# Optimization experiments

Hardware: AMD Instinct MI355X
Metric: run time of the kernel (lower is better)

The kernel has to match this reference:

```python
import jax, jax.numpy as jnp
import numpy as np

WS = 7          # window_size[0]
UP = 2          # hardcoded upscale
WS2 = WS * UP   # 14
NUM_HEADS = 6
DIM = 192
HEAD_DIM = DIM // NUM_HEADS
SCALE = HEAD_DIM ** -0.5
TABLE_SIZE = (WS + WS2 - 1) ** 2  # 400


def _relative_position_index():
    # Mirrors the torch __init__ index construction (meshgrid 'ij').
    ch = np.arange(WS)
    cw = np.arange(WS2)
    r1, c1 = np.meshgrid(ch, ch, indexing='ij')   # (7,7)
    r2, c2 = np.meshgrid(cw, cw, indexing='ij')   # (14,14)
    r1, c1 = r1.reshape(-1), c1.reshape(-1)       # (49,)
    r2, c2 = r2.reshape(-1), c2.reshape(-1)       # (196,)
    rel_row = r1[:, None] - r2[None, :] + (WS2 - 1)          # (49,196) in [0,19]
    rel_col = c1[:, None] - c2[None, :] + (WS2 - 1)
    idx = rel_row * (WS + WS2 - 1) + rel_col                 # (49,196) in [0,399]
    return jnp.asarray(idx, dtype=jnp.int32)

REL_INDEX = _relative_position_index()


def setup_inputs() -> dict:
    key = jax.random.key(0)
    ks = jax.random.split(key, 9)
    B, N, N2, C = 1024, WS * WS, WS2 * WS2, DIM
    std = 0.02
    return {
        'x1': jax.random.normal(ks[0], (B, N, C), jnp.float32),
        'x2': jax.random.normal(ks[1], (B, N2, C), jnp.float32),
        # Linear weights stored as (in, out) so y = x @ W + b
        'qkv_w': jax.random.normal(ks[2], (C, C), jnp.float32) * std,
        'qkv_b': jnp.zeros((C,), jnp.float32),
        'qkv2_w': jax.random.normal(ks[3], (C, 2 * C), jnp.float32) * std,
        'qkv2_b': jnp.zeros((2 * C,), jnp.float32),
        'proj_w': jax.random.normal(ks[4], (C, C), jnp.float32) * std,
        'proj_b': jnp.zeros((C,), jnp.float32),
        'bias_table': jax.random.normal(ks[5], (TABLE_SIZE, NUM_HEADS), jnp.float32) * std,
    }


def reference(x1, x2, qkv_w, qkv_b, qkv2_w, qkv2_b, proj_w, proj_b, bias_table):
    B, N, C = x1.shape
    _, N2, _ = x2.shape
    H, D = NUM_HEADS, HEAD_DIM

    q = (x1 @ qkv_w + qkv_b).reshape(B, N, H, D).transpose(0, 2, 1, 3)        # [B,H,N,D]
    kv = (x2 @ qkv2_w + qkv2_b).reshape(B, N2, 2, H, D).transpose(2, 0, 3, 1, 4)
    k, v = kv[0], kv[1]                                                        # [B,H,N2,D]

    attn = jnp.einsum('bhnd,bhmd->bhnm', q * SCALE, k)                         # [B,H,N,N2]
    bias = bias_table[REL_INDEX].transpose(2, 0, 1)                            # [H,N,N2]
    attn = jax.nn.softmax(attn + bias[None], axis=-1)

    out = jnp.einsum('bhnm,bhmd->bhnd', attn, v).transpose(0, 2, 1, 3).reshape(B, N, C)
    return out @ proj_w + proj_b
```

## Files before the change

### kernel.cpp

```cpp
#include <hip/hip_runtime.h>


typedef __attribute__((ext_vector_type(8))) short bf16x8;
typedef __attribute__((ext_vector_type(4))) float f32x4;

#define MFMA16(a, b, c) __builtin_amdgcn_mfma_f32_16x16x32_bf16((a), (b), (c), 0, 0, 0)

#define WS_QKVT  0
#define WS_QKV2T 36864
#define WS_PROJH 110592
#define WS_PROJL 147456

#define SCALE_Q 0.17677669529663687f

__device__ __forceinline__ unsigned short f2bf(float f) {
  unsigned int u = __float_as_uint(f);
  u += 0x7fffu + ((u >> 16) & 1u);
  return (unsigned short)(u >> 16);
}
__device__ __forceinline__ float bf2f(unsigned short s) {
  return __uint_as_float(((unsigned int)s) << 16);
}
__device__ __forceinline__ bf16x8 cvt8(const float* __restrict__ p) {
  union { bf16x8 v; unsigned short s[8]; } U;
  float4 v0 = *(const float4*)p;
  float4 v1 = *(const float4*)(p + 4);
  U.s[0] = f2bf(v0.x); U.s[1] = f2bf(v0.y); U.s[2] = f2bf(v0.z); U.s[3] = f2bf(v0.w);
  U.s[4] = f2bf(v1.x); U.s[5] = f2bf(v1.y); U.s[6] = f2bf(v1.z); U.s[7] = f2bf(v1.w);
  return U.v;
}

__global__ void prep_kernel(const float* __restrict__ qkv_w,
                            const float* __restrict__ qkv2_w,
                            const float* __restrict__ proj_w,
                            unsigned short* __restrict__ ws) {
  int t = blockIdx.x * 256 + threadIdx.x;
  if (t < 36864) {
    int k = t / 192, n = t % 192;
    ws[WS_QKVT + n * 192 + k] = f2bf(qkv_w[t]);
  } else if (t < 110592) {
    int u = t - 36864;
    int k = u / 384, n = u % 384;
    ws[WS_QKV2T + n * 192 + k] = f2bf(qkv2_w[u]);
  } else if (t < 147456) {
    int u = t - 110592;
    int k = u / 192, n = u % 192;
    float p = proj_w[u];
    unsigned short hi = f2bf(p);
    ws[WS_PROJH + n * 192 + k] = hi;
    ws[WS_PROJL + n * 192 + k] = f2bf(p - bf2f(hi));
  }
}

__launch_bounds__(256, 2)
__global__ void attn_kernel(const float* __restrict__ x1,
                            const float* __restrict__ x2,
                            const float* __restrict__ qkv_b,
                            const float* __restrict__ qkv2_b,
                            const float* __restrict__ btab,
                            const unsigned short* __restrict__ ws,
                            float* __restrict__ out) {
  extern __shared__ char smem[];
  unsigned short* ksm = (unsigned short*)(smem);
  unsigned short* vtm = (unsigned short*)(smem + 15680);
  unsigned short* atm = (unsigned short*)(smem + 30528);
  unsigned short* qhm = (unsigned short*)(smem + 60224);

  const int tid  = threadIdx.x;
  const int wave = tid >> 6;
  const int lane = tid & 63;
  const int l16  = lane & 15;
  const int quad = lane >> 4;
  const int b    = blockIdx.x;

  const float* x1b = x1 + (size_t)b * (49 * 192);
  const float* x2b = x2 + (size_t)b * (196 * 192);

  {
    int* z = (int*)(smem + 30528);
    for (int i = tid; i < 29696 / 4; i += 256) z[i] = 0;
    int* z2 = (int*)(smem + 15680);
    for (int i = tid; i < 14848 / 4; i += 256) z2[i] = 0;
  }

  int Pr6[4];
#pragma unroll
  for (int r = 0; r < 4; ++r) {
    int i = wave * 16 + quad * 4 + r;
    if (i > 48) i = 48;
    int ih = i / 7, iw = i - 7 * ih;
    Pr6[r] = (ih * 20 + iw + 273) * 6;
  }
  int qj6[13];
#pragma unroll
  for (int nt = 0; nt < 13; ++nt) {
    int jc = nt * 16 + l16;
    if (jc > 195) jc = 195;
    int jh = jc / 14, jw = jc - 14 * jh;
    qj6[nt] = (jh * 20 + jw) * 6;
  }

  bf16x8 x1f[6];
  {
    const int m = wave * 16 + l16;
    const bool mv = (m < 49);
#pragma unroll
    for (int kk = 0; kk < 6; ++kk) {
      if (mv) x1f[kk] = cvt8(x1b + m * 192 + kk * 32 + quad * 8);
      else    x1f[kk] = bf16x8{0, 0, 0, 0, 0, 0, 0, 0};
    }
  }
  bf16x8 x2f[3][6];
#pragma unroll
  for (int ti = 0; ti < 3; ++ti) {
    const int m = (wave + ti * 4) * 16 + l16;
#pragma unroll
    for (int kk = 0; kk < 6; ++kk)
      x2f[ti][kk] = cvt8(x2b + m * 192 + kk * 32 + quad * 8);
  }

  __syncthreads();

  for (int h = 0; h < 6; ++h) {
    {
      f32x4 acc0{0.f, 0.f, 0.f, 0.f}, acc1{0.f, 0.f, 0.f, 0.f};
#pragma unroll
      for (int kk = 0; kk < 6; ++kk) {
        const unsigned short* wq = ws + WS_QKVT + (h * 32 + l16) * 192 + kk * 32 + quad * 8;
        acc0 = MFMA16(x1f[kk], *(const bf16x8*)(wq), acc0);
        acc1 = MFMA16(x1f[kk], *(const bf16x8*)(wq + 16 * 192), acc1);
      }
      const float bia0 = qkv_b[h * 32 + l16];
      const float bia1 = qkv_b[h * 32 + 16 + l16];
#pragma unroll
      for (int r = 0; r < 4; ++r) {
        const int row = wave * 16 + quad * 4 + r;
        qhm[row * 40 + l16]      = f2bf((acc0[r] + bia0) * SCALE_Q);
        qhm[row * 40 + 16 + l16] = f2bf((acc1[r] + bia1) * SCALE_Q);
      }
    }
    const float bk0 = qkv2_b[h * 32 + l16];
    const float bk1 = qkv2_b[h * 32 + 16 + l16];
    const float bv0 = qkv2_b[192 + h * 32 + l16];
    const float bv1 = qkv2_b[192 + h * 32 + 16 + l16];
#pragma unroll
    for (int ti = 0; ti < 3; ++ti) {
      const int mt = wave + ti * 4;
      f32x4 acc0{0.f, 0.f, 0.f, 0.f}, acc1{0.f, 0.f, 0.f, 0.f};
      f32x4 acc2{0.f, 0.f, 0.f, 0.f}, acc3{0.f, 0.f, 0.f, 0.f};
#pragma unroll
      for (int kk = 0; kk < 6; ++kk) {
        const unsigned short* wk = ws + WS_QKV2T + (h * 32 + l16) * 192 + kk * 32 + quad * 8;
        acc0 = MFMA16(x2f[ti][kk], *(const bf16x8*)(wk), acc0);
        acc1 = MFMA16(x2f[ti][kk], *(const bf16x8*)(wk + 16 * 192), acc1);
        acc2 = MFMA16(x2f[ti][kk], *(const bf16x8*)(wk + 192 * 192), acc2);
        acc3 = MFMA16(x2f[ti][kk], *(const bf16x8*)(wk + 208 * 192), acc3);
      }
#pragma unroll
      for (int r = 0; r < 4; ++r) {
        const int row = mt * 16 + quad * 4 + r;
        ksm[row * 40 + l16]      = f2bf(acc0[r] + bk0);
        ksm[row * 40 + 16 + l16] = f2bf(acc1[r] + bk1);
        vtm[l16 * 232 + row]        = f2bf(acc2[r] + bv0);
        vtm[(16 + l16) * 232 + row] = f2bf(acc3[r] + bv1);
      }
    }
    if (wave == 0) {
      f32x4 acc0{0.f, 0.f, 0.f, 0.f}, acc1{0.f, 0.f, 0.f, 0.f};
      f32x4 acc2{0.f, 0.f, 0.f, 0.f}, acc3{0.f, 0.f, 0.f, 0.f};
      const int m = 192 + l16;
      const bool mv = (m < 196);
#pragma unroll
      for (int kk = 0; kk < 6; ++kk) {
        const int k0 = kk * 32 + quad * 8;
        bf16x8 a;
        if (mv) a = cvt8(x2b + m * 192 + k0);
        else    a = bf16x8{0, 0, 0, 0, 0, 0, 0, 0};
        const unsigned short* wk = ws + WS_QKV2T + (h * 32 + l16) * 192 + k0;
        acc0 = MFMA16(a, *(const bf16x8*)(wk), acc0);
        acc1 = MFMA16(a, *(const bf16x8*)(wk + 16 * 192), acc1);
        acc2 = MFMA16(a, *(const bf16x8*)(wk + 192 * 192), acc2);
        acc3 = MFMA16(a, *(const bf16x8*)(wk + 208 * 192), acc3);
      }
#pragma unroll
      for (int r = 0; r < 4; ++r) {
        const int row = 192 + quad * 4 + r;
        if (row < 196) {
          ksm[row * 40 + l16]      = f2bf(acc0[r] + bk0);
          ksm[row * 40 + 16 + l16] = f2bf(acc1[r] + bk1);
        }
        vtm[l16 * 232 + row]        = f2bf(acc2[r] + bv0);
        vtm[(16 + l16) * 232 + row] = f2bf(acc3[r] + bv1);
      }
    }
    __syncthreads();

    f32x4 lg[13];
    {
      const int m = wave * 16 + l16;
      bf16x8 a = *(const bf16x8*)(qhm + m * 40 + quad * 8);
#pragma unroll
      for (int nt = 0; nt < 12; ++nt) {
#pragma unroll
        for (int r = 0; r < 4; ++r) lg[nt][r] = btab[Pr6[r] - qj6[nt] + h];
      }
#pragma unroll
      for (int r = 0; r < 4; ++r)
        lg[12][r] = (l16 < 4) ? btab[Pr6[r] - qj6[12] + h] : -1e30f;
#pragma unroll
      for (int nt = 0; nt < 13; ++nt) {
        bf16x8 bb = *(const bf16x8*)(ksm + (nt * 16 + l16) * 40 + quad * 8);
        lg[nt] = MFMA16(a, bb, lg[nt]);
      }
#pragma unroll
      for (int r = 0; r < 4; ++r) {
        float mx = lg[0][r];
#pragma unroll
        for (int nt = 1; nt < 13; ++nt) mx = fmaxf(mx, lg[nt][r]);
        mx = fmaxf(mx, __shfl_xor(mx, 1));
        mx = fmaxf(mx, __shfl_xor(mx, 2));
        mx = fmaxf(mx, __shfl_xor(mx, 4));
        mx = fmaxf(mx, __shfl_xor(mx, 8));
        float s = 0.f;
#pragma unroll
        for (int nt = 0; nt < 13; ++nt) {
          float p = __expf(lg[nt][r] - mx);
          lg[nt][r] = p;
          s += p;
        }
        s += __shfl_xor(s, 1);
        s += __shfl_xor(s, 2);
        s += __shfl_xor(s, 4);
        s += __shfl_xor(s, 8);
        const float inv = 1.f / s;
        const int row = wave * 16 + quad * 4 + r;
        if (row < 49) {
#pragma unroll
          for (int nt = 0; nt < 13; ++nt)
            atm[row * 232 + nt * 16 + l16] = f2bf(lg[nt][r] * inv);
        }
      }
    }
    {
      f32x4 o0{0.f, 0.f, 0.f, 0.f}, o1{0.f, 0.f, 0.f, 0.f};
      const int m = wave * 16 + l16;
#pragma unroll
      for (int kk = 0; kk < 7; ++kk) {
        const int k0 = kk * 32 + quad * 8;
        bf16x8 a  = *(const bf16x8*)(atm + m * 232 + k0);
        bf16x8 b0 = *(const bf16x8*)(vtm + l16 * 232 + k0);
        bf16x8 b1 = *(const bf16x8*)(vtm + (16 + l16) * 232 + k0);
        o0 = MFMA16(a, b0, o0);
        o1 = MFMA16(a, b1, o1);
      }
#pragma unroll
      for (int r = 0; r < 4; ++r) {
        const int row = wave * 16 + quad * 4 + r;
        if (row < 49) {
          float* op = out + (size_t)b * 9408 + row * 192 + h * 32;
          op[l16]      = o0[r];
          op[16 + l16] = o1[r];
        }
      }
    }
    __syncthreads();
  }
}

__launch_bounds__(256, 2)
__global__ void proj_kernel(const float* __restrict__ proj_b,
                            const unsigned short* __restrict__ ws,
                            float* __restrict__ out) {
  extern __shared__ char smem[];
  float* aout = (float*)smem;
  const int tid  = threadIdx.x;
  const int wave = tid >> 6;
  const int lane = tid & 63;
  const int l16  = lane & 15;
  const int quad = lane >> 4;
  const size_t base = (size_t)blockIdx.x * 64 * 192;

  for (int i = tid; i < 64 * 192 / 4; i += 256) {
    int row = i / 48, col = (i - row * 48) * 4;
    float4 v = *(const float4*)(out + base + row * 192 + col);
    *(float4*)(aout + row * 204 + col) = v;
  }
  __syncthreads();

  f32x4 pacc[12];
#pragma unroll
  for (int nt = 0; nt < 12; ++nt) pacc[nt] = f32x4{0.f, 0.f, 0.f, 0.f};

  const int m = wave * 16 + l16;
#pragma unroll
  for (int kk = 0; kk < 6; ++kk) {
    const int k0 = kk * 32 + quad * 8;
    const float* ap = aout + m * 204 + k0;
    float4 v0 = *(const float4*)ap;
    float4 v1 = *(const float4*)(ap + 4);
    float f[8] = {v0.x, v0.y, v0.z, v0.w, v1.x, v1.y, v1.z, v1.w};
    union { bf16x8 v; unsigned short s[8]; } H, L;
#pragma unroll
    for (int j = 0; j < 8; ++j) {
      H.s[j] = f2bf(f[j]);
      L.s[j] = f2bf(f[j] - bf2f(H.s[j]));
    }
#pragma unroll
    for (int nt = 0; nt < 12; ++nt) {
      const unsigned short* bph = ws + WS_PROJH + (nt * 16 + l16) * 192 + k0;
      const unsigned short* bpl = ws + WS_PROJL + (nt * 16 + l16) * 192 + k0;
      bf16x8 bh = *(const bf16x8*)bph;
      bf16x8 bl = *(const bf16x8*)bpl;
      pacc[nt] = MFMA16(H.v, bh, pacc[nt]);
      pacc[nt] = MFMA16(H.v, bl, pacc[nt]);
      pacc[nt] = MFMA16(L.v, bh, pacc[nt]);
    }
  }
#pragma unroll
  for (int nt = 0; nt < 12; ++nt) {
    const float pb = proj_b[nt * 16 + l16];
#pragma unroll
    for (int r = 0; r < 4; ++r) {
      const int row = wave * 16 + quad * 4 + r;
      out[base + row * 192 + nt * 16 + l16] = pacc[nt][r] + pb;
    }
  }
}

extern "C" void kernel_launch(void* const* d_in, const int* in_sizes, int n_in,
                              void* d_out, int out_size, void* d_ws, size_t ws_size,
                              hipStream_t stream) {
  const float* x1     = (const float*)d_in[0];
  const float* x2     = (const float*)d_in[1];
  const float* qkv_w  = (const float*)d_in[2];
  const float* qkv_b  = (const float*)d_in[3];
  const float* qkv2_w = (const float*)d_in[4];
  const float* qkv2_b = (const float*)d_in[5];
  const float* proj_w = (const float*)d_in[6];
  const float* proj_b = (const float*)d_in[7];
  const float* btab   = (const float*)d_in[8];
  unsigned short* ws  = (unsigned short*)d_ws;
  float* out          = (float*)d_out;
  (void)in_sizes; (void)n_in; (void)out_size; (void)ws_size;

  prep_kernel<<<dim3(576), dim3(256), 0, stream>>>(qkv_w, qkv2_w, proj_w, ws);
  attn_kernel<<<dim3(1024), dim3(256), 65344, stream>>>(x1, x2, qkv_b, qkv2_b,
                                                        btab, ws, out);
  proj_kernel<<<dim3(784), dim3(256), 52224, stream>>>(proj_b, ws, out);
}
```

Baseline: 704.1 us.

## Split fused attention into QKV projection and per-head attention kernels via workspace

When the workspace is large enough, the single fused attention kernel is replaced by a QKV projection kernel that writes bf16 Q, K and transposed V to global memory. A separate attention kernel then assigns one wave per (window, head) and uses a precomputed padded bias table as the initial logits. The proj kernel now reads its activations directly from global memory without LDS staging, so it can run at higher occupancy. The split is meant to raise parallelism and occupancy, at the cost of extra global memory round-trips for Q, K and V (roughly hundreds of MB of workspace).

```diff
diff --git a/kernel.cpp b/kernel.cpp
--- a/kernel.cpp
+++ b/kernel.cpp
@@ -10,6 +10,11 @@
 #define WS_QKV2T 36864
 #define WS_PROJH 110592
 #define WS_PROJL 147456
+#define BIAS_F32 92160
+#define QG_U16   524288
+#define KG_U16   13107200
+#define VTG_U16  54001664
+#define WS_NEEDED 196083712ull
 
 #define SCALE_Q 0.17677669529663687f
 
@@ -33,6 +38,7 @@
 __global__ void prep_kernel(const float* __restrict__ qkv_w,
                             const float* __restrict__ qkv2_w,
                             const float* __restrict__ proj_w,
+                            const float* __restrict__ btab,
                             unsigned short* __restrict__ ws) {
   int t = blockIdx.x * 256 + threadIdx.x;
   if (t < 36864) {
@@ -49,6 +55,219 @@
     unsigned short hi = f2bf(p);
     ws[WS_PROJH + n * 192 + k] = hi;
     ws[WS_PROJL + n * 192 + k] = f2bf(p - bf2f(hi));
+  } else if (t < 233472) {
+    int u = t - 147456;
+    int h = u / 14336;
+    int r2 = u - h * 14336;
+    int key = r2 >> 6, qrow = r2 & 63;
+    float v;
+    if (key >= 196)      v = -1e30f;
+    else if (qrow >= 49) v = 0.f;
+    else {
+      int jh = key / 14, jw = key - 14 * jh;
+      int ih = qrow / 7, iw = qrow - 7 * ih;
+      v = btab[((ih - jh + 13) * 20 + (iw - jw + 13)) * 6 + h];
+    }
+    ((float*)ws)[BIAS_F32 + u] = v;
+  }
+}
+
+__launch_bounds__(256, 2)
+__global__ void qkv_kernel(const float* __restrict__ x1,
+                           const float* __restrict__ x2,
+                           const float* __restrict__ qkv_b,
+                           const float* __restrict__ qkv2_b,
+                           unsigned short* __restrict__ ws) {
+  const int tid  = threadIdx.x;
+  const int wave = tid >> 6;
+  const int lane = tid & 63;
+  const int l16  = lane & 15;
+  const int quad = lane >> 4;
+  const int b    = blockIdx.x;
+
+  const float* x1b = x1 + (size_t)b * (49 * 192);
+  const float* x2b = x2 + (size_t)b * (196 * 192);
+  unsigned short* qg = ws + QG_U16  + (size_t)b * 6 * 2048;
+  unsigned short* kg = ws + KG_U16  + (size_t)b * 6 * 6656;
+  unsigned short* vg = ws + VTG_U16 + (size_t)b * 6 * 7168;
+
+  for (int i = tid; i < 1536; i += 256) {
+    int hh = i >> 8, j = i & 255;
+    *(unsigned int*)(vg + hh * 7168 + (j >> 3) * 224 + 208 + (j & 7) * 2) = 0u;
+  }
+
+  bf16x8 x1f[6];
+  {
+    const int m = wave * 16 + l16;
+    const bool mv = (m < 49);
+#pragma unroll
+    for (int kk = 0; kk < 6; ++kk)
+      x1f[kk] = mv ? cvt8(x1b + m * 192 + kk * 32 + quad * 8)
+                   : bf16x8{0, 0, 0, 0, 0, 0, 0, 0};
+  }
+  bf16x8 x2f[3][6];
+#pragma unroll
+  for (int ti = 0; ti < 3; ++ti) {
+    const int m = (wave + ti * 4) * 16 + l16;
+#pragma unroll
+    for (int kk = 0; kk < 6; ++kk)
+      x2f[ti][kk] = cvt8(x2b + m * 192 + kk * 32 + quad * 8);
+  }
+
+  for (int h = 0; h < 6; ++h) {
+    {
+      f32x4 a0{0.f, 0.f, 0.f, 0.f}, a1{0.f, 0.f, 0.f, 0.f};
+#pragma unroll
+      for (int kk = 0; kk < 6; ++kk) {
+        const unsigned short* wq = ws + WS_QKVT + (h * 32 + l16) * 192 + kk * 32 + quad * 8;
+        a0 = MFMA16(x1f[kk], *(const bf16x8*)(wq), a0);
+        a1 = MFMA16(x1f[kk], *(const bf16x8*)(wq + 16 * 192), a1);
+      }
+      const float b0 = qkv_b[h * 32 + l16];
+      const float b1 = qkv_b[h * 32 + 16 + l16];
+      unsigned short* qh = qg + h * 2048;
+#pragma unroll
+      for (int r = 0; r < 4; ++r) {
+        const int row = wave * 16 + quad * 4 + r;
+        qh[row * 32 + l16]      = f2bf((a0[r] + b0) * SCALE_Q);
+        qh[row * 32 + 16 + l16] = f2bf((a1[r] + b1) * SCALE_Q);
+      }
+    }
+    const float bk0 = qkv2_b[h * 32 + l16];
+    const float bk1 = qkv2_b[h * 32 + 16 + l16];
+    const float bv0 = qkv2_b[192 + h * 32 + l16];
+    const float bv1 = qkv2_b[192 + h * 32 + 16 + l16];
+    unsigned short* kh = kg + h * 6656;
+    unsigned short* vh = vg + h * 7168;
+#pragma unroll
+    for (int ti = 0; ti < 3; ++ti) {
+      const int mt = wave + ti * 4;
+      f32x4 a0{0.f, 0.f, 0.f, 0.f}, a1{0.f, 0.f, 0.f, 0.f};
+      f32x4 a2{0.f, 0.f, 0.f, 0.f}, a3{0.f, 0.f, 0.f, 0.f};
+#pragma unroll
+      for (int kk = 0; kk < 6; ++kk) {
+        const unsigned short* wk = ws + WS_QKV2T + (h * 32 + l16) * 192 + kk * 32 + quad * 8;
+        a0 = MFMA16(x2f[ti][kk], *(const bf16x8*)(wk), a0);
+        a1 = MFMA16(x2f[ti][kk], *(const bf16x8*)(wk + 16 * 192), a1);
+        a2 = MFMA16(x2f[ti][kk], *(const bf16x8*)(wk + 192 * 192), a2);
+        a3 = MFMA16(x2f[ti][kk], *(const bf16x8*)(wk + 208 * 192), a3);
+      }
+#pragma unroll
+      for (int r = 0; r < 4; ++r) {
+        const int row = mt * 16 + quad * 4 + r;
+        kh[row * 32 + l16]        = f2bf(a0[r] + bk0);
+        kh[row * 32 + 16 + l16]   = f2bf(a1[r] + bk1);
+        vh[l16 * 224 + row]       = f2bf(a2[r] + bv0);
+        vh[(16 + l16) * 224 + row] = f2bf(a3[r] + bv1);
+      }
+    }
+    if (wave == 0) {
+      f32x4 a0{0.f, 0.f, 0.f, 0.f}, a1{0.f, 0.f, 0.f, 0.f};
+      f32x4 a2{0.f, 0.f, 0.f, 0.f}, a3{0.f, 0.f, 0.f, 0.f};
+      const int m = 192 + l16;
+      const bool mv = (m < 196);
+#pragma unroll
+      for (int kk = 0; kk < 6; ++kk) {
+        bf16x8 a = mv ? cvt8(x2b + m * 192 + kk * 32 + quad * 8)
+                      : bf16x8{0, 0, 0, 0, 0, 0, 0, 0};
+        const unsigned short* wk = ws + WS_QKV2T + (h * 32 + l16) * 192 + kk * 32 + quad * 8;
+        a0 = MFMA16(a, *(const bf16x8*)(wk), a0);
+        a1 = MFMA16(a, *(const bf16x8*)(wk + 16 * 192), a1);
+        a2 = MFMA16(a, *(const bf16x8*)(wk + 192 * 192), a2);
+        a3 = MFMA16(a, *(const bf16x8*)(wk + 208 * 192), a3);
+      }
+#pragma unroll
+      for (int r = 0; r < 4; ++r) {
+        const int row = 192 + quad * 4 + r;
+        const bool rv = (row < 196);
+        kh[row * 32 + l16]        = rv ? f2bf(a0[r] + bk0) : (unsigned short)0;
+        kh[row * 32 + 16 + l16]   = rv ? f2bf(a1[r] + bk1) : (unsigned short)0;
+        vh[l16 * 224 + row]       = rv ? f2bf(a2[r] + bv0) : (unsigned short)0;
+        vh[(16 + l16) * 224 + row] = rv ? f2bf(a3[r] + bv1) : (unsigned short)0;
+      }
+    }
+  }
+}
+
+__launch_bounds__(256, 4)
+__global__ void attn2_kernel(const unsigned short* __restrict__ ws,
+                             float* __restrict__ out) {
+  __shared__ unsigned short ps4[4][16 * 232];
+  const int tid  = threadIdx.x;
+  const int wave = tid >> 6;
+  const int lane = tid & 63;
+  const int l16  = lane & 15;
+  const int quad = lane >> 4;
+  const int wid  = blockIdx.x * 4 + wave;
+  const int win  = wid / 6, head = wid - win * 6;
+
+  const unsigned short* qb = ws + QG_U16  + (size_t)wid * 2048;
+  const unsigned short* kb = ws + KG_U16  + (size_t)wid * 6656;
+  const unsigned short* vb = ws + VTG_U16 + (size_t)wid * 7168;
+  const float* bbt = (const float*)ws + BIAS_F32 + head * 14336;
+  unsigned short* ps = ps4[wave];
+  float* ob = out + (size_t)win * 9408 + head * 32;
+
+  for (int i = lane; i < 192; i += 64) {
+    int rr = i / 12, cc = (i - rr * 12) * 2;
+    *(unsigned int*)(ps + rr * 232 + 208 + cc) = 0u;
+  }
+
+  for (int mt = 0; mt < 4; ++mt) {
+    bf16x8 aq = *(const bf16x8*)(qb + (mt * 16 + l16) * 32 + quad * 8);
+    f32x4 lg[13];
+#pragma unroll
+    for (int nt = 0; nt < 13; ++nt)
+      lg[nt] = *(const f32x4*)(bbt + (nt * 16 + l16) * 64 + mt * 16 + quad * 4);
+#pragma unroll
+    for (int nt = 0; nt < 13; ++nt)
+      lg[nt] = MFMA16(aq, *(const bf16x8*)(kb + (nt * 16 + l16) * 32 + quad * 8), lg[nt]);
+
+#pragma unroll
+    for (int r = 0; r < 4; ++r) {
+      float mx = lg[0][r];
+#pragma unroll
+      for (int nt = 1; nt < 13; ++nt) mx = fmaxf(mx, lg[nt][r]);
+      mx = fmaxf(mx, __shfl_xor(mx, 1));
+      mx = fmaxf(mx, __shfl_xor(mx, 2));
+      mx = fmaxf(mx, __shfl_xor(mx, 4));
+      mx = fmaxf(mx, __shfl_xor(mx, 8));
+      float s = 0.f;
+#pragma unroll
+      for (int nt = 0; nt < 13; ++nt) {
+        float p = __expf(lg[nt][r] - mx);
+        lg[nt][r] = p;
+        s += p;
+      }
+      s += __shfl_xor(s, 1);
+      s += __shfl_xor(s, 2);
+      s += __shfl_xor(s, 4);
+      s += __shfl_xor(s, 8);
+      const float inv = 1.f / s;
+      const int row = quad * 4 + r;
+#pragma unroll
+      for (int nt = 0; nt < 13; ++nt)
+        ps[row * 232 + nt * 16 + l16] = f2bf(lg[nt][r] * inv);
+    }
+
+    f32x4 o0{0.f, 0.f, 0.f, 0.f}, o1{0.f, 0.f, 0.f, 0.f};
+#pragma unroll
+    for (int kk = 0; kk < 7; ++kk) {
+      bf16x8 a  = *(const bf16x8*)(ps + l16 * 232 + kk * 32 + quad * 8);
+      bf16x8 b0 = *(const bf16x8*)(vb + l16 * 224 + kk * 32 + quad * 8);
+      bf16x8 b1 = *(const bf16x8*)(vb + (16 + l16) * 224 + kk * 32 + quad * 8);
+      o0 = MFMA16(a, b0, o0);
+      o1 = MFMA16(a, b1, o1);
+    }
+#pragma unroll
+    for (int r = 0; r < 4; ++r) {
+      const int row = mt * 16 + quad * 4 + r;
+      if (row < 49) {
+        float* op = ob + row * 192;
+        op[l16]      = o0[r];
+        op[16 + l16] = o1[r];
+      }
+    }
   }
 }
 
@@ -267,12 +486,10 @@
   }
 }
 
-__launch_bounds__(256, 2)
+__launch_bounds__(256, 4)
 __global__ void proj_kernel(const float* __restrict__ proj_b,
                             const unsigned short* __restrict__ ws,
                             float* __restrict__ out) {
-  extern __shared__ char smem[];
-  float* aout = (float*)smem;
   const int tid  = threadIdx.x;
   const int wave = tid >> 6;
   const int lane = tid & 63;
@@ -280,24 +497,17 @@
   const int quad = lane >> 4;
   const size_t base = (size_t)blockIdx.x * 64 * 192;
 
-  for (int i = tid; i < 64 * 192 / 4; i += 256) {
-    int row = i / 48, col = (i - row * 48) * 4;
-    float4 v = *(const float4*)(out + base + row * 192 + col);
-    *(float4*)(aout + row * 204 + col) = v;
-  }
-  __syncthreads();
-
   f32x4 pacc[12];
 #pragma unroll
   for (int nt = 0; nt < 12; ++nt) pacc[nt] = f32x4{0.f, 0.f, 0.f, 0.f};
 
   const int m = wave * 16 + l16;
+  const float* ap0 = out + base + m * 192;
 #pragma unroll
   for (int kk = 0; kk < 6; ++kk) {
     const int k0 = kk * 32 + quad * 8;
-    const float* ap = aout + m * 204 + k0;
-    float4 v0 = *(const float4*)ap;
-    float4 v1 = *(const float4*)(ap + 4);
+    float4 v0 = *(const float4*)(ap0 + k0);
+    float4 v1 = *(const float4*)(ap0 + k0 + 4);
     float f[8] = {v0.x, v0.y, v0.z, v0.w, v1.x, v1.y, v1.z, v1.w};
     union { bf16x8 v; unsigned short s[8]; } H, L;
 #pragma unroll
@@ -307,10 +517,8 @@
     }
 #pragma unroll
     for (int nt = 0; nt < 12; ++nt) {
-      const unsigned short* bph = ws + WS_PROJH + (nt * 16 + l16) * 192 + k0;
-      const unsigned short* bpl = ws + WS_PROJL + (nt * 16 + l16) * 192 + k0;
-      bf16x8 bh = *(const bf16x8*)bph;
-      bf16x8 bl = *(const bf16x8*)bpl;
+      bf16x8 bh = *(const bf16x8*)(ws + WS_PROJH + (nt * 16 + l16) * 192 + k0);
+      bf16x8 bl = *(const bf16x8*)(ws + WS_PROJL + (nt * 16 + l16) * 192 + k0);
       pacc[nt] = MFMA16(H.v, bh, pacc[nt]);
       pacc[nt] = MFMA16(H.v, bl, pacc[nt]);
       pacc[nt] = MFMA16(L.v, bh, pacc[nt]);
@@ -341,10 +549,17 @@
   const float* btab   = (const float*)d_in[8];
   unsigned short* ws  = (unsigned short*)d_ws;
   float* out          = (float*)d_out;
-  (void)in_sizes; (void)n_in; (void)out_size; (void)ws_size;
-
-  prep_kernel<<<dim3(576), dim3(256), 0, stream>>>(qkv_w, qkv2_w, proj_w, ws);
-  attn_kernel<<<dim3(1024), dim3(256), 65344, stream>>>(x1, x2, qkv_b, qkv2_b,
-                                                        btab, ws, out);
-  proj_kernel<<<dim3(784), dim3(256), 52224, stream>>>(proj_b, ws, out);
-}
+  (void)in_sizes; (void)n_in; (void)out_size;
+
+  if (ws_size >= WS_NEEDED) {
+    prep_kernel<<<dim3(912), dim3(256), 0, stream>>>(qkv_w, qkv2_w, proj_w, btab, ws);
+    qkv_kernel<<<dim3(1024), dim3(256), 0, stream>>>(x1, x2, qkv_b, qkv2_b, ws);
+    attn2_kernel<<<dim3(1536), dim3(256), 0, stream>>>(ws, out);
+    proj_kernel<<<dim3(784), dim3(256), 0, stream>>>(proj_b, ws, out);
+  } else {
+    prep_kernel<<<dim3(576), dim3(256), 0, stream>>>(qkv_w, qkv2_w, proj_w, btab, ws);
+    attn_kernel<<<dim3(1024), dim3(256), 65344, stream>>>(x1, x2, qkv_b, qkv2_b,
+                                                          btab, ws, out);
+    proj_kernel<<<dim3(784), dim3(256), 0, stream>>>(proj_b, ws, out);
+  }
+}
```

Result: slower. 813.6 us (+15.5%).

## Split attention per window-head block, precompute dense bias table, shrink proj tiles

Applied to the files above, without the earlier changes.

The attention kernel now launches one block per (window, head) pair instead of looping over the six heads inside one block per window. Blocks are ordered so that neighbouring block IDs map to different windows. Shared memory drops to a static 36 KB, so occupancy can rise to four blocks per CU. The relative-position bias is expanded once in the prep kernel into a dense, padded fp32 table per head, which gives vectorised bias loads instead of per-element gathers. The proj kernel handles 32 rows per block and reads directly from global memory without LDS staging. In exchange, x1 and x2 are reread and converted to bf16 six times per window, and each attention block launches with fewer waves of useful work.

```diff
diff --git a/kernel.cpp b/kernel.cpp
--- a/kernel.cpp
+++ b/kernel.cpp
@@ -10,6 +10,7 @@
 #define WS_QKV2T 36864
 #define WS_PROJH 110592
 #define WS_PROJL 147456
+#define BIAS_F32 92160
 
 #define SCALE_Q 0.17677669529663687f
 
@@ -33,6 +34,7 @@
 __global__ void prep_kernel(const float* __restrict__ qkv_w,
                             const float* __restrict__ qkv2_w,
                             const float* __restrict__ proj_w,
+                            const float* __restrict__ btab,
                             unsigned short* __restrict__ ws) {
   int t = blockIdx.x * 256 + threadIdx.x;
   if (t < 36864) {
@@ -49,255 +51,247 @@
     unsigned short hi = f2bf(p);
     ws[WS_PROJH + n * 192 + k] = hi;
     ws[WS_PROJL + n * 192 + k] = f2bf(p - bf2f(hi));
-  }
-}
-
-__launch_bounds__(256, 2)
-__global__ void attn_kernel(const float* __restrict__ x1,
-                            const float* __restrict__ x2,
-                            const float* __restrict__ qkv_b,
-                            const float* __restrict__ qkv2_b,
-                            const float* __restrict__ btab,
-                            const unsigned short* __restrict__ ws,
-                            float* __restrict__ out) {
-  extern __shared__ char smem[];
+  } else if (t < 233472) {
+    int u = t - 147456;
+    int h = u / 14336;
+    int r2 = u - h * 14336;
+    int key = r2 >> 6, qrow = r2 & 63;
+    float v;
+    if (key >= 196)      v = -1e30f;
+    else if (qrow >= 49) v = 0.f;
+    else {
+      int jh = key / 14, jw = key - 14 * jh;
+      int ih = qrow / 7, iw = qrow - 7 * ih;
+      v = btab[((ih - jh + 13) * 20 + (iw - jw + 13)) * 6 + h];
+    }
+    ((float*)ws)[BIAS_F32 + u] = v;
+  }
+}
+
+__launch_bounds__(256, 4)
+__global__ void fused_attn_kernel(const float* __restrict__ x1,
+                                  const float* __restrict__ x2,
+                                  const float* __restrict__ qkv_b,
+                                  const float* __restrict__ qkv2_b,
+                                  const unsigned short* __restrict__ ws,
+                                  float* __restrict__ out) {
+  __shared__ __align__(16) char smem[36608];
   unsigned short* ksm = (unsigned short*)(smem);
-  unsigned short* vtm = (unsigned short*)(smem + 15680);
-  unsigned short* atm = (unsigned short*)(smem + 30528);
-  unsigned short* qhm = (unsigned short*)(smem + 60224);
+  unsigned short* qhm = (unsigned short*)(smem + 16640);
+  unsigned short* vtm = (unsigned short*)(smem + 21760);
 
   const int tid  = threadIdx.x;
   const int wave = tid >> 6;
   const int lane = tid & 63;
   const int l16  = lane & 15;
   const int quad = lane >> 4;
-  const int b    = blockIdx.x;
-
-  const float* x1b = x1 + (size_t)b * (49 * 192);
-  const float* x2b = x2 + (size_t)b * (196 * 192);
-
-  {
-    int* z = (int*)(smem + 30528);
-    for (int i = tid; i < 29696 / 4; i += 256) z[i] = 0;
-    int* z2 = (int*)(smem + 15680);
-    for (int i = tid; i < 14848 / 4; i += 256) z2[i] = 0;
-  }
-
-  int Pr6[4];
+
+  const int logical = (blockIdx.x & 7) * 768 + (blockIdx.x >> 3);
+  const int win  = logical / 6;
+  const int h    = logical - win * 6;
+
+  const float* x1b = x1 + (size_t)win * (49 * 192);
+  const float* x2b = x2 + (size_t)win * (196 * 192);
+  const float* bbt = (const float*)ws + BIAS_F32 + h * 14336;
+
+  {
+    int d = tid >> 3, c = tid & 7;
+    *(unsigned int*)(vtm + d * 232 + 208 + c * 2) = 0u;
+  }
+
+  {
+    f32x4 qa0{0.f, 0.f, 0.f, 0.f}, qa1{0.f, 0.f, 0.f, 0.f};
+    const int mq = wave * 16 + l16;
+    const bool mv = (mq < 49);
+#pragma unroll
+    for (int kk = 0; kk < 6; ++kk) {
+      bf16x8 a = mv ? cvt8(x1b + mq * 192 + kk * 32 + quad * 8)
+                    : bf16x8{0, 0, 0, 0, 0, 0, 0, 0};
+      const unsigned short* wq = ws + WS_QKVT + (h * 32 + l16) * 192 + kk * 32 + quad * 8;
+      qa0 = MFMA16(a, *(const bf16x8*)(wq), qa0);
+      qa1 = MFMA16(a, *(const bf16x8*)(wq + 16 * 192), qa1);
+    }
+    const float b0 = qkv_b[h * 32 + l16];
+    const float b1 = qkv_b[h * 32 + 16 + l16];
+#pragma unroll
+    for (int r = 0; r < 4; ++r) {
+      const int row = wave * 16 + quad * 4 + r;
+      qhm[row * 40 + l16]      = f2bf((qa0[r] + b0) * SCALE_Q);
+      qhm[row * 40 + 16 + l16] = f2bf((qa1[r] + b1) * SCALE_Q);
+    }
+  }
+  const float bk0 = qkv2_b[h * 32 + l16];
+  const float bk1 = qkv2_b[h * 32 + 16 + l16];
+  const float bv0 = qkv2_b[192 + h * 32 + l16];
+  const float bv1 = qkv2_b[192 + h * 32 + 16 + l16];
+  {
+    f32x4 ka0[3], ka1[3], va0[3], va1[3];
+#pragma unroll
+    for (int ti = 0; ti < 3; ++ti) {
+      ka0[ti] = f32x4{0.f, 0.f, 0.f, 0.f}; ka1[ti] = f32x4{0.f, 0.f, 0.f, 0.f};
+      va0[ti] = f32x4{0.f, 0.f, 0.f, 0.f}; va1[ti] = f32x4{0.f, 0.f, 0.f, 0.f};
+    }
+#pragma unroll 2
+    for (int kk = 0; kk < 6; ++kk) {
+      const unsigned short* wk = ws + WS_QKV2T + (h * 32 + l16) * 192 + kk * 32 + quad * 8;
+      bf16x8 w0 = *(const bf16x8*)(wk);
+      bf16x8 w1 = *(const bf16x8*)(wk + 16 * 192);
+      bf16x8 w2 = *(const bf16x8*)(wk + 192 * 192);
+      bf16x8 w3 = *(const bf16x8*)(wk + 208 * 192);
+#pragma unroll
+      for (int ti = 0; ti < 3; ++ti) {
+        bf16x8 a = cvt8(x2b + ((ti * 4 + wave) * 16 + l16) * 192 + kk * 32 + quad * 8);
+        ka0[ti] = MFMA16(a, w0, ka0[ti]);
+        ka1[ti] = MFMA16(a, w1, ka1[ti]);
+        va0[ti] = MFMA16(a, w2, va0[ti]);
+        va1[ti] = MFMA16(a, w3, va1[ti]);
+      }
+    }
+#pragma unroll
+    for (int ti = 0; ti < 3; ++ti) {
+#pragma unroll
+      for (int r = 0; r < 4; ++r) {
+        const int row = (ti * 4 + wave) * 16 + quad * 4 + r;
+        ksm[row * 40 + l16]        = f2bf(ka0[ti][r] + bk0);
+        ksm[row * 40 + 16 + l16]   = f2bf(ka1[ti][r] + bk1);
+        vtm[l16 * 232 + row]        = f2bf(va0[ti][r] + bv0);
+        vtm[(16 + l16) * 232 + row] = f2bf(va1[ti][r] + bv1);
+      }
+    }
+  }
+  if (wave == 0) {
+    f32x4 a0{0.f, 0.f, 0.f, 0.f}, a1{0.f, 0.f, 0.f, 0.f};
+    f32x4 a2{0.f, 0.f, 0.f, 0.f}, a3{0.f, 0.f, 0.f, 0.f};
+    const int m = 192 + l16;
+    const bool mv = (m < 196);
+#pragma unroll 2
+    for (int kk = 0; kk < 6; ++kk) {
+      bf16x8 a = mv ? cvt8(x2b + m * 192 + kk * 32 + quad * 8)
+                    : bf16x8{0, 0, 0, 0, 0, 0, 0, 0};
+      const unsigned short* wk = ws + WS_QKV2T + (h * 32 + l16) * 192 + kk * 32 + quad * 8;
+      a0 = MFMA16(a, *(const bf16x8*)(wk), a0);
+      a1 = MFMA16(a, *(const bf16x8*)(wk + 16 * 192), a1);
+      a2 = MFMA16(a, *(const bf16x8*)(wk + 192 * 192), a2);
+      a3 = MFMA16(a, *(const bf16x8*)(wk + 208 * 192), a3);
+    }
+#pragma unroll
+    for (int r = 0; r < 4; ++r) {
+      const int row = 192 + quad * 4 + r;
+      const bool rv = (row < 196);
+      ksm[row * 40 + l16]        = rv ? f2bf(a0[r] + bk0) : (unsigned short)0;
+      ksm[row * 40 + 16 + l16]   = rv ? f2bf(a1[r] + bk1) : (unsigned short)0;
+      vtm[l16 * 232 + row]        = rv ? f2bf(a2[r] + bv0) : (unsigned short)0;
+      vtm[(16 + l16) * 232 + row] = rv ? f2bf(a3[r] + bv1) : (unsigned short)0;
+    }
+  }
+  __syncthreads();
+
+  f32x4 lg[13];
+  {
+    bf16x8 aq = *(const bf16x8*)(qhm + (wave * 16 + l16) * 40 + quad * 8);
+#pragma unroll
+    for (int nt = 0; nt < 13; ++nt)
+      lg[nt] = *(const f32x4*)(bbt + (nt * 16 + l16) * 64 + wave * 16 + quad * 4);
+#pragma unroll
+    for (int nt = 0; nt < 13; ++nt)
+      lg[nt] = MFMA16(aq, *(const bf16x8*)(ksm + (nt * 16 + l16) * 40 + quad * 8), lg[nt]);
+#pragma unroll
+    for (int r = 0; r < 4; ++r) {
+      float mx = lg[0][r];
+#pragma unroll
+      for (int nt = 1; nt < 13; ++nt) mx = fmaxf(mx, lg[nt][r]);
+      mx = fmaxf(mx, __shfl_xor(mx, 1));
+      mx = fmaxf(mx, __shfl_xor(mx, 2));
+      mx = fmaxf(mx, __shfl_xor(mx, 4));
+      mx = fmaxf(mx, __shfl_xor(mx, 8));
+      float s = 0.f;
+#pragma unroll
+      for (int nt = 0; nt < 13; ++nt) {
+        float p = __expf(lg[nt][r] - mx);
+        lg[nt][r] = p;
+        s += p;
+      }
+      s += __shfl_xor(s, 1);
+      s += __shfl_xor(s, 2);
+      s += __shfl_xor(s, 4);
+      s += __shfl_xor(s, 8);
+      const float inv = 1.f / s;
+#pragma unroll
+      for (int nt = 0; nt < 13; ++nt) lg[nt][r] *= inv;
+    }
+  }
+  __syncthreads();
+
+  unsigned short* ps = (unsigned short*)(smem + wave * 4352);
+  f32x4 o0{0.f, 0.f, 0.f, 0.f}, o1{0.f, 0.f, 0.f, 0.f};
 #pragma unroll
   for (int r = 0; r < 4; ++r) {
-    int i = wave * 16 + quad * 4 + r;
-    if (i > 48) i = 48;
-    int ih = i / 7, iw = i - 7 * ih;
-    Pr6[r] = (ih * 20 + iw + 273) * 6;
-  }
-  int qj6[13];
-#pragma unroll
-  for (int nt = 0; nt < 13; ++nt) {
-    int jc = nt * 16 + l16;
-    if (jc > 195) jc = 195;
-    int jh = jc / 14, jw = jc - 14 * jh;
-    qj6[nt] = (jh * 20 + jw) * 6;
-  }
-
-  bf16x8 x1f[6];
-  {
-    const int m = wave * 16 + l16;
-    const bool mv = (m < 49);
-#pragma unroll
-    for (int kk = 0; kk < 6; ++kk) {
-      if (mv) x1f[kk] = cvt8(x1b + m * 192 + kk * 32 + quad * 8);
-      else    x1f[kk] = bf16x8{0, 0, 0, 0, 0, 0, 0, 0};
-    }
-  }
-  bf16x8 x2f[3][6];
-#pragma unroll
-  for (int ti = 0; ti < 3; ++ti) {
-    const int m = (wave + ti * 4) * 16 + l16;
-#pragma unroll
-    for (int kk = 0; kk < 6; ++kk)
-      x2f[ti][kk] = cvt8(x2b + m * 192 + kk * 32 + quad * 8);
-  }
-
-  __syncthreads();
-
-  for (int h = 0; h < 6; ++h) {
-    {
-      f32x4 acc0{0.f, 0.f, 0.f, 0.f}, acc1{0.f, 0.f, 0.f, 0.f};
-#pragma unroll
-      for (int kk = 0; kk < 6; ++kk) {
-        const unsigned short* wq = ws + WS_QKVT + (h * 32 + l16) * 192 + kk * 32 + quad * 8;
-        acc0 = MFMA16(x1f[kk], *(const bf16x8*)(wq), acc0);
-        acc1 = MFMA16(x1f[kk], *(const bf16x8*)(wq + 16 * 192), acc1);
+    const int row = quad * 4 + r;
+#pragma unroll
+    for (int nt = 0; nt < 8; ++nt)
+      ps[row * 136 + nt * 16 + l16] = f2bf(lg[nt][r]);
+  }
+#pragma unroll
+  for (int kk = 0; kk < 4; ++kk) {
+    bf16x8 a  = *(const bf16x8*)(ps + l16 * 136 + kk * 32 + quad * 8);
+    bf16x8 b0 = *(const bf16x8*)(vtm + l16 * 232 + kk * 32 + quad * 8);
+    bf16x8 b1 = *(const bf16x8*)(vtm + (16 + l16) * 232 + kk * 32 + quad * 8);
+    o0 = MFMA16(a, b0, o0);
+    o1 = MFMA16(a, b1, o1);
+  }
+#pragma unroll
+  for (int r = 0; r < 4; ++r) {
+    const int row = quad * 4 + r;
+#pragma unroll
+    for (int nt = 8; nt < 13; ++nt)
+      ps[row * 104 + (nt - 8) * 16 + l16] = f2bf(lg[nt][r]);
+    ps[row * 104 + 80 + l16] = 0;
+  }
+#pragma unroll
+  for (int kk = 0; kk < 3; ++kk) {
+    bf16x8 a  = *(const bf16x8*)(ps + l16 * 104 + kk * 32 + quad * 8);
+    bf16x8 b0 = *(const bf16x8*)(vtm + l16 * 232 + (4 + kk) * 32 + quad * 8);
+    bf16x8 b1 = *(const bf16x8*)(vtm + (16 + l16) * 232 + (4 + kk) * 32 + quad * 8);
+    o0 = MFMA16(a, b0, o0);
+    o1 = MFMA16(a, b1, o1);
+  }
+  {
+    float* ob = out + (size_t)win * 9408 + h * 32;
+#pragma unroll
+    for (int r = 0; r < 4; ++r) {
+      const int row = wave * 16 + quad * 4 + r;
+      if (row < 49) {
+        float* op = ob + row * 192;
+        op[l16]      = o0[r];
+        op[16 + l16] = o1[r];
       }
-      const float bia0 = qkv_b[h * 32 + l16];
-      const float bia1 = qkv_b[h * 32 + 16 + l16];
-#pragma unroll
-      for (int r = 0; r < 4; ++r) {
-        const int row = wave * 16 + quad * 4 + r;
-        qhm[row * 40 + l16]      = f2bf((acc0[r] + bia0) * SCALE_Q);
-        qhm[row * 40 + 16 + l16] = f2bf((acc1[r] + bia1) * SCALE_Q);
-      }
-    }
-    const float bk0 = qkv2_b[h * 32 + l16];
-    const float bk1 = qkv2_b[h * 32 + 16 + l16];
-    const float bv0 = qkv2_b[192 + h * 32 + l16];
-    const float bv1 = qkv2_b[192 + h * 32 + 16 + l16];
-#pragma unroll
-    for (int ti = 0; ti < 3; ++ti) {
-      const int mt = wave + ti * 4;
-      f32x4 acc0{0.f, 0.f, 0.f, 0.f}, acc1{0.f, 0.f, 0.f, 0.f};
-      f32x4 acc2{0.f, 0.f, 0.f, 0.f}, acc3{0.f, 0.f, 0.f, 0.f};
-#pragma unroll
-      for (int kk = 0; kk < 6; ++kk) {
-        const unsigned short* wk = ws + WS_QKV2T + (h * 32 + l16) * 192 + kk * 32 + quad * 8;
-        acc0 = MFMA16(x2f[ti][kk], *(const bf16x8*)(wk), acc0);
-        acc1 = MFMA16(x2f[ti][kk], *(const bf16x8*)(wk + 16 * 192), acc1);
-        acc2 = MFMA16(x2f[ti][kk], *(const bf16x8*)(wk + 192 * 192), acc2);
-        acc3 = MFMA16(x2f[ti][kk], *(const bf16x8*)(wk + 208 * 192), acc3);
-      }
-#pragma unroll
-      for (int r = 0; r < 4; ++r) {
-        const int row = mt * 16 + quad * 4 + r;
-        ksm[row * 40 + l16]      = f2bf(acc0[r] + bk0);
-        ksm[row * 40 + 16 + l16] = f2bf(acc1[r] + bk1);
-        vtm[l16 * 232 + row]        = f2bf(acc2[r] + bv0);
-        vtm[(16 + l16) * 232 + row] = f2bf(acc3[r] + bv1);
-      }
-    }
-    if (wave == 0) {
-      f32x4 acc0{0.f, 0.f, 0.f, 0.f}, acc1{0.f, 0.f, 0.f, 0.f};
-      f32x4 acc2{0.f, 0.f, 0.f, 0.f}, acc3{0.f, 0.f, 0.f, 0.f};
-      const int m = 192 + l16;
-      const bool mv = (m < 196);
-#pragma unroll
-      for (int kk = 0; kk < 6; ++kk) {
-        const int k0 = kk * 32 + quad * 8;
-        bf16x8 a;
-        if (mv) a = cvt8(x2b + m * 192 + k0);
-        else    a = bf16x8{0, 0, 0, 0, 0, 0, 0, 0};
-        const unsigned short* wk = ws + WS_QKV2T + (h * 32 + l16) * 192 + k0;
-        acc0 = MFMA16(a, *(const bf16x8*)(wk), acc0);
-        acc1 = MFMA16(a, *(const bf16x8*)(wk + 16 * 192), acc1);
-        acc2 = MFMA16(a, *(const bf16x8*)(wk + 192 * 192), acc2);
-        acc3 = MFMA16(a, *(const bf16x8*)(wk + 208 * 192), acc3);
-      }
-#pragma unroll
-      for (int r = 0; r < 4; ++r) {
-        const int row = 192 + quad * 4 + r;
-        if (row < 196) {
-          ksm[row * 40 + l16]      = f2bf(acc0[r] + bk0);
-          ksm[row * 40 + 16 + l16] = f2bf(acc1[r] + bk1);
-        }
-        vtm[l16 * 232 + row]        = f2bf(acc2[r] + bv0);
-        vtm[(16 + l16) * 232 + row] = f2bf(acc3[r] + bv1);
-      }
-    }
-    __syncthreads();
-
-    f32x4 lg[13];
-    {
-      const int m = wave * 16 + l16;
-      bf16x8 a = *(const bf16x8*)(qhm + m * 40 + quad * 8);
-#pragma unroll
-      for (int nt = 0; nt < 12; ++nt) {
-#pragma unroll
-        for (int r = 0; r < 4; ++r) lg[nt][r] = btab[Pr6[r] - qj6[nt] + h];
-      }
-#pragma unroll
-      for (int r = 0; r < 4; ++r)
-        lg[12][r] = (l16 < 4) ? btab[Pr6[r] - qj6[12] + h] : -1e30f;
-#pragma unroll
-      for (int nt = 0; nt < 13; ++nt) {
-        bf16x8 bb = *(const bf16x8*)(ksm + (nt * 16 + l16) * 40 + quad * 8);
-        lg[nt] = MFMA16(a, bb, lg[nt]);
-      }
-#pragma unroll
-      for (int r = 0; r < 4; ++r) {
-        float mx = lg[0][r];
-#pragma unroll
-        for (int nt = 1; nt < 13; ++nt) mx = fmaxf(mx, lg[nt][r]);
-        mx = fmaxf(mx, __shfl_xor(mx, 1));
-        mx = fmaxf(mx, __shfl_xor(mx, 2));
-        mx = fmaxf(mx, __shfl_xor(mx, 4));
-        mx = fmaxf(mx, __shfl_xor(mx, 8));
-        float s = 0.f;
-#pragma unroll
-        for (int nt = 0; nt < 13; ++nt) {
-          float p = __expf(lg[nt][r] - mx);
-          lg[nt][r] = p;
-          s += p;
-        }
-        s += __shfl_xor(s, 1);
-        s += __shfl_xor(s, 2);
-        s += __shfl_xor(s, 4);
-        s += __shfl_xor(s, 8);
-        const float inv = 1.f / s;
-        const int row = wave * 16 + quad * 4 + r;
-        if (row < 49) {
-#pragma unroll
-          for (int nt = 0; nt < 13; ++nt)
-            atm[row * 232 + nt * 16 + l16] = f2bf(lg[nt][r] * inv);
-        }
-      }
-    }
-    {
-      f32x4 o0{0.f, 0.f, 0.f, 0.f}, o1{0.f, 0.f, 0.f, 0.f};
-      const int m = wave * 16 + l16;
-#pragma unroll
-      for (int kk = 0; kk < 7; ++kk) {
-        const int k0 = kk * 32 + quad * 8;
-        bf16x8 a  = *(const bf16x8*)(atm + m * 232 + k0);
-        bf16x8 b0 = *(const bf16x8*)(vtm + l16 * 232 + k0);
-        bf16x8 b1 = *(const bf16x8*)(vtm + (16 + l16) * 232 + k0);
-        o0 = MFMA16(a, b0, o0);
-        o1 = MFMA16(a, b1, o1);
-      }
-#pragma unroll
-      for (int r = 0; r < 4; ++r) {
-        const int row = wave * 16 + quad * 4 + r;
-        if (row < 49) {
-          float* op = out + (size_t)b * 9408 + row * 192 + h * 32;
-          op[l16]      = o0[r];
-          op[16 + l16] = o1[r];
-        }
-      }
-    }
-    __syncthreads();
-  }
-}
-
-__launch_bounds__(256, 2)
+    }
+  }
+}
+
+__launch_bounds__(256, 4)
 __global__ void proj_kernel(const float* __restrict__ proj_b,
                             const unsigned short* __restrict__ ws,
                             float* __restrict__ out) {
-  extern __shared__ char smem[];
-  float* aout = (float*)smem;
   const int tid  = threadIdx.x;
   const int wave = tid >> 6;
   const int lane = tid & 63;
   const int l16  = lane & 15;
   const int quad = lane >> 4;
-  const size_t base = (size_t)blockIdx.x * 64 * 192;
-
-  for (int i = tid; i < 64 * 192 / 4; i += 256) {
-    int row = i / 48, col = (i - row * 48) * 4;
-    float4 v = *(const float4*)(out + base + row * 192 + col);
-    *(float4*)(aout + row * 204 + col) = v;
-  }
-  __syncthreads();
-
-  f32x4 pacc[12];
-#pragma unroll
-  for (int nt = 0; nt < 12; ++nt) pacc[nt] = f32x4{0.f, 0.f, 0.f, 0.f};
-
-  const int m = wave * 16 + l16;
-#pragma unroll
+  const int rowg = (wave & 1) * 16;
+  const int nth  = (wave >> 1) * 6;
+  const size_t base = (size_t)blockIdx.x * 32 * 192;
+
+  f32x4 pacc[6];
+#pragma unroll
+  for (int nt = 0; nt < 6; ++nt) pacc[nt] = f32x4{0.f, 0.f, 0.f, 0.f};
+
+  const float* ap0 = out + base + (rowg + l16) * 192;
+#pragma unroll 2
   for (int kk = 0; kk < 6; ++kk) {
     const int k0 = kk * 32 + quad * 8;
-    const float* ap = aout + m * 204 + k0;
-    float4 v0 = *(const float4*)ap;
-    float4 v1 = *(const float4*)(ap + 4);
+    float4 v0 = *(const float4*)(ap0 + k0);
+    float4 v1 = *(const float4*)(ap0 + k0 + 4);
     float f[8] = {v0.x, v0.y, v0.z, v0.w, v1.x, v1.y, v1.z, v1.w};
     union { bf16x8 v; unsigned short s[8]; } H, L;
 #pragma unroll
@@ -306,23 +300,22 @@
       L.s[j] = f2bf(f[j] - bf2f(H.s[j]));
     }
 #pragma unroll
-    for (int nt = 0; nt < 12; ++nt) {
-      const unsigned short* bph = ws + WS_PROJH + (nt * 16 + l16) * 192 + k0;
-      const unsigned short* bpl = ws + WS_PROJL + (nt * 16 + l16) * 192 + k0;
-      bf16x8 bh = *(const bf16x8*)bph;
-      bf16x8 bl = *(const bf16x8*)bpl;
+    for (int nt = 0; nt < 6; ++nt) {
+      bf16x8 bh = *(const bf16x8*)(ws + WS_PROJH + ((nth + nt) * 16 + l16) * 192 + k0);
+      bf16x8 bl = *(const bf16x8*)(ws + WS_PROJL + ((nth + nt) * 16 + l16) * 192 + k0);
       pacc[nt] = MFMA16(H.v, bh, pacc[nt]);
       pacc[nt] = MFMA16(H.v, bl, pacc[nt]);
       pacc[nt] = MFMA16(L.v, bh, pacc[nt]);
     }
   }
-#pragma unroll
-  for (int nt = 0; nt < 12; ++nt) {
-    const float pb = proj_b[nt * 16 + l16];
-#pragma unroll
-    for (int r = 0; r < 4; ++r) {
-      const int row = wave * 16 + quad * 4 + r;
-      out[base + row * 192 + nt * 16 + l16] = pacc[nt][r] + pb;
+  __syncthreads();
+#pragma unroll
+  for (int nt = 0; nt < 6; ++nt) {
+    const float pb = proj_b[(nth + nt) * 16 + l16];
+#pragma unroll
+    for (int r = 0; r < 4; ++r) {
+      const int row = rowg + quad * 4 + r;
+      out[base + row * 192 + (nth + nt) * 16 + l16] = pacc[nt][r] + pb;
     }
   }
 }
@@ -343,8 +336,8 @@
   float* out          = (float*)d_out;
   (void)in_sizes; (void)n_in; (void)out_size; (void)ws_size;
 
-  prep_kernel<<<dim3(576), dim3(256), 0, stream>>>(qkv_w, qkv2_w, proj_w, ws);
-  attn_kernel<<<dim3(1024), dim3(256), 65344, stream>>>(x1, x2, qkv_b, qkv2_b,
-                                                        btab, ws, out);
-  proj_kernel<<<dim3(784), dim3(256), 52224, stream>>>(proj_b, ws, out);
-}
+  prep_kernel<<<dim3(912), dim3(256), 0, stream>>>(qkv_w, qkv2_w, proj_w, btab, ws);
+  fused_attn_kernel<<<dim3(6144), dim3(256), 0, stream>>>(x1, x2, qkv_b, qkv2_b,
+                                                          ws, out);
+  proj_kernel<<<dim3(1568), dim3(256), 0, stream>>>(proj_b, ws, out);
+}
```

After: 574.7 us. -18.4%, faster.
